# Performance work log

Hardware: AMD Instinct MI355X
Metric: run time of the kernel (lower is better)

Reference implementation:

```python
import jax, jax.numpy as jnp
import numpy as np

NBINS = 256
EARLY_STOP = 0.1  # fraction of nbins with no improvement before early break


def setup_inputs() -> dict:
    key = jax.random.key(0)
    x = jax.random.uniform(key, (8, 3, 1024, 1024), dtype=jnp.float32)
    return {"x": x}


def _otsu_forward(x):
    orig_shape = x.shape
    b, c, h, w = x.shape
    rows = b * c
    xf = x.reshape(rows, h * w)                      # (R, N) one image per row
    N = xf.shape[1]

    # Per-row shift so each row starts at 0 (mirrors `x = (x.T - min_value).T`).
    min_val = xf.min(axis=1, keepdims=True)          # (R, 1)
    xs = xf - min_val
    gmax = xs.max()                                  # global min of xs is 0, global max here
    edges = jnp.linspace(jnp.zeros((), xs.dtype), gmax, NBINS + 1)
    width = gmax / NBINS

    # Per-row histogram with torch.histc semantics over global [0, gmax].
    bin_idx = jnp.clip(jnp.floor(xs / width).astype(jnp.int32), 0, NBINS - 1)
    flat_idx = (jnp.arange(rows, dtype=jnp.int32)[:, None] * NBINS + bin_idx).reshape(-1)
    hist = jnp.bincount(flat_idx, length=rows * NBINS).reshape(rows, NBINS).astype(xs.dtype)
    cum_count = jnp.cumsum(hist, axis=1)             # px_bellow after each bin
    w0 = cum_count / N
    w1 = 1.0 - w0

    # Sorted prefix moments -> subset variances for every threshold in one pass.
    xsort = jnp.sort(xs, axis=1)
    row_mean = xs.mean(axis=1, keepdims=True)
    cvals = xsort - row_mean                         # variance is shift-invariant; centering for stability
    s1 = jnp.cumsum(cvals, axis=1)
    s2 = jnp.cumsum(cvals * cvals, axis=1)
    tot1 = s1[:, -1:]
    tot2 = s2[:, -1:]

    thresh = edges[1:]                               # bin_edges[bin+1], shape (NBINS,)
    # n0[r, bin] = #{xs[r] <= thresh[bin]}  (condition `x <= thresh` in the loop)
    n0 = jax.vmap(lambda row: jnp.searchsorted(row, thresh, side="right"))(xsort)  # (R, NBINS)

    def subset_var(S1, S2, n):
        # unbiased variance (torch.var default); nan for n <= 1 like torch
        nf = n.astype(xs.dtype)
        var = (S2 - S1 * S1 / jnp.maximum(nf, 1.0)) / jnp.maximum(nf - 1.0, 1.0)
        return jnp.where(n > 1, var, jnp.nan)

    idx0 = jnp.maximum(n0 - 1, 0)
    S1_0 = jnp.where(n0 > 0, jnp.take_along_axis(s1, idx0, axis=1), 0.0)
    S2_0 = jnp.where(n0 > 0, jnp.take_along_axis(s2, idx0, axis=1), 0.0)
    mu0 = subset_var(S1_0, S2_0, n0)                 # var of pixels <= thresh
    n1 = N - n0
    mu1 = subset_var(tot1 - S1_0, tot2 - S2_0, n1)   # var of pixels > thresh
    icv = w0 * w1 * (mu0 - mu1) ** 2                 # (R, NBINS)

    # Sequential argmax with the original's global early-stop counter.
    max_try = int(NBINS * EARLY_STOP)

    def step(carry, inputs):
        max_icv, best, no_upd, stopped = carry
        icv_b, t_b = inputs                          # (R,), scalar
        upd = (icv_b > max_icv) & jnp.logical_not(stopped)   # nan > x is False, as in torch
        max_icv = jnp.where(upd, icv_b, max_icv)
        best = jnp.where(upd, t_b, best)
        no_upd = jnp.where(jnp.any(upd), 0, no_upd + 1)
        stopped = stopped | (no_upd >= max_try)
        return (max_icv, best, no_upd, stopped), None

    init = (
        jnp.zeros(rows, xs.dtype),
        jnp.zeros(rows, xs.dtype),
        jnp.zeros((), jnp.int32),
        jnp.zeros((), jnp.bool_),
    )
    (_, best_thresh, _, _), _ = jax.lax.scan(step, init, (icv.T, thresh))

    final_thresh = best_thresh[:, None] + min_val    # back to original scale
    out = jnp.where(xf < final_thresh, jnp.zeros((), xs.dtype), xf)
    return out.reshape(orig_shape)


def reference(x):
    return _otsu_forward(x)
```

## Files before the change

### kernel.cpp

```cpp
#include <hip/hip_runtime.h>
#include <stdint.h>


#define ROWS 24
#define NPIX (1 << 20)
#define NBINS 256
#define BPR 64
#define CHUNK (NPIX / BPR)
#define MAX_TRY 25

static constexpr double kScale = 1099511627776.0;
static constexpr double Nd = 1048576.0;

#define OFF_MINNOT 0
#define OFF_MAXB   128
#define OFF_FINAL  256
#define OFF_CNT    512
#define OFF_COR    (OFF_CNT + ROWS*NBINS*4)
#define OFF_S1     (OFF_COR + ROWS*NBINS*4)
#define OFF_S2     (OFF_S1 + ROWS*NBINS*8)
#define WS_TOTAL   (OFF_S2 + ROWS*NBINS*8)

__device__ __forceinline__ double wave_gmax(const unsigned* __restrict__ minnot,
                                            const unsigned* __restrict__ maxb,
                                            int lane) {
  double d = 0.0;
  if (lane < ROWS) {
    d = (double)__uint_as_float(maxb[lane]) - (double)__uint_as_float(~minnot[lane]);
  }
  for (int o = 16; o; o >>= 1) d = fmax(d, __shfl_down(d, o));
  return d;
}

__global__ __launch_bounds__(256) void k_minmax(const float* __restrict__ x,
                                                unsigned* __restrict__ minnot,
                                                unsigned* __restrict__ maxb) {
  int row = blockIdx.x / BPR;
  int sub = blockIdx.x % BPR;
  const float4* p = (const float4*)(x + (size_t)row * NPIX + (size_t)sub * CHUNK);
  float mn = 3.4e38f, mx = 0.0f;
  for (int i = threadIdx.x; i < CHUNK / 4; i += 256) {
    float4 v = p[i];
    mn = fminf(mn, fminf(fminf(v.x, v.y), fminf(v.z, v.w)));
    mx = fmaxf(mx, fmaxf(fmaxf(v.x, v.y), fmaxf(v.z, v.w)));
  }
  __shared__ float smn[4], smx[4];
  for (int o = 32; o; o >>= 1) {
    mn = fminf(mn, __shfl_down(mn, o));
    mx = fmaxf(mx, __shfl_down(mx, o));
  }
  int wave = threadIdx.x >> 6;
  if ((threadIdx.x & 63) == 0) { smn[wave] = mn; smx[wave] = mx; }
  __syncthreads();
  if (threadIdx.x == 0) {
    for (int w = 1; w < 4; ++w) { mn = fminf(mn, smn[w]); mx = fmaxf(mx, smx[w]); }
    atomicMax(&minnot[row], ~__float_as_uint(mn));
    atomicMax(&maxb[row], __float_as_uint(mx));
  }
}

__global__ __launch_bounds__(256) void k_hist(const float* __restrict__ x,
    const unsigned* __restrict__ minnot, const unsigned* __restrict__ maxb,
    unsigned* __restrict__ gcnt, int* __restrict__ gcor,
    unsigned long long* __restrict__ gs1, unsigned long long* __restrict__ gs2) {
  __shared__ unsigned hc[NBINS];
  __shared__ int hcor[NBINS];
  __shared__ unsigned long long h1[NBINS], h2[NBINS];
  __shared__ double s_w, s_rmin;
  int t = threadIdx.x;
  hc[t] = 0u; hcor[t] = 0; h1[t] = 0ull; h2[t] = 0ull;
  int row = blockIdx.x / BPR;
  int sub = blockIdx.x % BPR;
  if (t < 64) {
    double g = wave_gmax(minnot, maxb, t);
    if (t == 0) {
      s_w = g / 256.0;
      s_rmin = (double)__uint_as_float(~minnot[row]);
    }
  }
  __syncthreads();
  double w = s_w, rmin = s_rmin;
  const float4* p = (const float4*)(x + (size_t)row * NPIX + (size_t)sub * CHUNK);
  for (int i = threadIdx.x; i < CHUNK / 4; i += 256) {
    float4 v = p[i];
    float vv[4] = {v.x, v.y, v.z, v.w};
#pragma unroll
    for (int c = 0; c < 4; ++c) {
      double xs = (double)vv[c] - rmin;
      double q = xs / w;
      int b = (int)q;
      b = b > 255 ? 255 : b;
      double elo = (double)b * w;
      double ehi = (double)(b + 1) * w;
      int j = b;
      if (xs > ehi) { if (b < 255) j = b + 1; }
      else if (b > 0 && xs <= elo) j = b - 1;
      atomicAdd(&hc[j], 1u);
      if (j != b) {
        atomicAdd(&hcor[b], 1);
        atomicAdd(&hcor[j], -1);
      }
      unsigned long long a1 = (unsigned long long)llrint(xs * kScale);
      unsigned long long a2 = (unsigned long long)llrint(xs * xs * kScale);
      atomicAdd(&h1[j], a1);
      atomicAdd(&h2[j], a2);
    }
  }
  __syncthreads();
  atomicAdd(&gcnt[row * NBINS + t], hc[t]);
  if (hcor[t] != 0) atomicAdd(&gcor[row * NBINS + t], hcor[t]);
  atomicAdd(&gs1[row * NBINS + t], h1[t]);
  atomicAdd(&gs2[row * NBINS + t], h2[t]);
}

__global__ __launch_bounds__(1024) void k_icv_scan(
    const unsigned* __restrict__ gcnt, const int* __restrict__ gcor,
    const unsigned long long* __restrict__ gs1,
    const unsigned long long* __restrict__ gs2,
    const unsigned* __restrict__ minnot, const unsigned* __restrict__ maxb,
    double* __restrict__ finalt) {
  __shared__ double sicv[ROWS * NBINS];
  __shared__ double s_w;
  int tid = threadIdx.x;
  int wave = tid >> 6, lane = tid & 63;
  if (tid < 64) {
    double g = wave_gmax(minnot, maxb, lane);
    if (tid == 0) s_w = g / 256.0;
  }
  __syncthreads();

  const double dNAN = __builtin_nan("");
#pragma unroll
  for (int pass = 0; pass < 2; ++pass) {
    int r = (pass == 0) ? wave : 16 + wave;
    if (pass == 1 && wave >= 8) break;
    int base = r * NBINS + lane * 4;
    unsigned cj[4]; int cr[4];
    *(uint4*)cj = *(const uint4*)&gcnt[base];
    *(int4*)cr = *(const int4*)&gcor[base];
    unsigned long long s1v[4], s2v[4];
#pragma unroll
    for (int k = 0; k < 4; ++k) { s1v[k] = gs1[base + k]; s2v[k] = gs2[base + k]; }
    unsigned long long P[4], A[4], B[4];
    unsigned long long rp = 0, ra = 0, rb = 0;
#pragma unroll
    for (int k = 0; k < 4; ++k) {
      unsigned cf = cj[k] + (unsigned)cr[k];
      rp += (unsigned long long)cj[k] | ((unsigned long long)cf << 32);
      ra += s1v[k]; rb += s2v[k];
      P[k] = rp; A[k] = ra; B[k] = rb;
    }
    unsigned long long tp = rp, ta = ra, tb = rb;
    for (int o = 1; o < 64; o <<= 1) {
      unsigned long long up = __shfl_up(tp, o);
      unsigned long long ua = __shfl_up(ta, o);
      unsigned long long ub = __shfl_up(tb, o);
      if (lane >= o) { tp += up; ta += ua; tb += ub; }
    }
    unsigned long long totP = __shfl(tp, 63);
    unsigned long long totA = __shfl(ta, 63);
    unsigned long long totB = __shfl(tb, 63);
    unsigned long long ep = tp - rp, ea = ta - ra, eb = tb - rb;

    double total1 = (double)totA / kScale;
    double total2 = (double)totB / kScale;
    double mean = total1 / Nd;
    double tot1 = total1 - Nd * mean;
    double tot2 = total2 - Nd * mean * mean;
    (void)totP;
#pragma unroll
    for (int k = 0; k < 4; ++k) {
      unsigned long long Pk = P[k] + ep;
      unsigned long long cjc = Pk & 0xffffffffull;
      unsigned long long cfc = Pk >> 32;
      double n0 = (double)cjc;
      double n1 = Nd - n0;
      double s1raw = (double)(A[k] + ea) / kScale;
      double s2raw = (double)(B[k] + eb) / kScale;
      double S1 = s1raw - n0 * mean;
      double S2 = s2raw - 2.0 * mean * s1raw + n0 * mean * mean;
      double mu0 = (cjc > 1ull) ? (S2 - S1 * S1 / n0) / (n0 - 1.0) : dNAN;
      double S1b = tot1 - S1, S2b = tot2 - S2;
      double mu1 = (n1 > 1.0) ? (S2b - S1b * S1b / n1) / (n1 - 1.0) : dNAN;
      double w0 = (double)cfc / Nd, w1 = 1.0 - w0;
      double dd = mu0 - mu1;
      sicv[r * NBINS + lane * 4 + k] = w0 * w1 * dd * dd;
    }
  }
  __syncthreads();

  if (tid < 64) {
    int r = tid;
    bool active = r < ROWS;
    double w = s_w;
    double maxicv = 0.0, best = 0.0;
    int no_upd = 0;
    bool stopped = false;
    for (int t = 0; t < NBINS; ++t) {
      double v = active ? sicv[r * NBINS + t] : -1.0;
      bool upd = active && !stopped && (v > maxicv);
      if (upd) { maxicv = v; best = (double)(t + 1) * w; }
      unsigned long long bal = __ballot(upd);
      if (bal != 0ull) no_upd = 0; else ++no_upd;
      if (no_upd >= MAX_TRY) stopped = true;
    }
    if (active) finalt[r] = best + (double)__uint_as_float(~minnot[r]);
  }
}

__global__ __launch_bounds__(256) void k_out(const float* __restrict__ x,
                                             const double* __restrict__ finalt,
                                             float* __restrict__ out) {
  size_t i = (size_t)blockIdx.x * blockDim.x + threadIdx.x;
  size_t stride = (size_t)gridDim.x * blockDim.x;
  const float4* xin = (const float4*)x;
  float4* o = (float4*)out;
  size_t n4 = (size_t)ROWS * NPIX / 4;
  for (; i < n4; i += stride) {
    int row = (int)(i >> 18);
    double ft = finalt[row];
    float4 v = xin[i];
    float4 rr;
    rr.x = ((double)v.x < ft) ? 0.0f : v.x;
    rr.y = ((double)v.y < ft) ? 0.0f : v.y;
    rr.z = ((double)v.z < ft) ? 0.0f : v.z;
    rr.w = ((double)v.w < ft) ? 0.0f : v.w;
    o[i] = rr;
  }
}

extern "C" void kernel_launch(void* const* d_in, const int* in_sizes, int n_in,
                              void* d_out, int out_size, void* d_ws, size_t ws_size,
                              hipStream_t stream) {
  const float* x = (const float*)d_in[0];
  float* out = (float*)d_out;
  char* ws = (char*)d_ws;
  unsigned* minnot = (unsigned*)(ws + OFF_MINNOT);
  unsigned* maxb = (unsigned*)(ws + OFF_MAXB);
  double* finalt = (double*)(ws + OFF_FINAL);
  unsigned* gcnt = (unsigned*)(ws + OFF_CNT);
  int* gcor = (int*)(ws + OFF_COR);
  unsigned long long* gs1 = (unsigned long long*)(ws + OFF_S1);
  unsigned long long* gs2 = (unsigned long long*)(ws + OFF_S2);

  hipMemsetAsync(d_ws, 0, WS_TOTAL, stream);
  k_minmax<<<ROWS * BPR, 256, 0, stream>>>(x, minnot, maxb);
  k_hist<<<ROWS * BPR, 256, 0, stream>>>(x, minnot, maxb, gcnt, gcor, gs1, gs2);
  k_icv_scan<<<1, 1024, 0, stream>>>(gcnt, gcor, gs1, gs2, minnot, maxb, finalt);
  k_out<<<3072, 256, 0, stream>>>(x, finalt, out);
}
```

Baseline: 139.6 us.

## Accumulate bin-offset moments with packed count, reciprocal divide, and split ICV kernel

The histogram kernel now accumulates each pixel's offset from its bin's lower edge instead of raw values. The count is packed into the high bits of the first-moment atomic, removing one shared atomic per pixel. The per-pixel double division is replaced by a reciprocal multiply with an FMA correction step. The ICV computation moves from one 1024-thread block into a 24-block kernel followed by a tiny scan kernel. This cuts shared-memory atomics and double divides in the hot loop, at the cost of one extra launch and a different fixed-point precision scheme that could risk overflow.

Result: no change. 137.1 us (-1.8%).

```diff
diff --git a/kernel.cpp b/kernel.cpp
--- a/kernel.cpp
+++ b/kernel.cpp
@@ -9,7 +9,10 @@
 #define CHUNK (NPIX / BPR)
 #define MAX_TRY 25
 
-static constexpr double kScale = 1099511627776.0;
+static constexpr double kD1Scale = 17592186044416.0;
+static constexpr double kD1Inv   = 1.0 / 17592186044416.0;
+static constexpr double kD2Scale = 4503599627370496.0;
+static constexpr double kD2Inv   = 1.0 / 4503599627370496.0;
 static constexpr double Nd = 1048576.0;
 
 #define OFF_MINNOT 0
@@ -17,9 +20,10 @@
 #define OFF_FINAL  256
 #define OFF_CNT    512
 #define OFF_COR    (OFF_CNT + ROWS*NBINS*4)
-#define OFF_S1     (OFF_COR + ROWS*NBINS*4)
-#define OFF_S2     (OFF_S1 + ROWS*NBINS*8)
-#define WS_TOTAL   (OFF_S2 + ROWS*NBINS*8)
+#define OFF_D1     (OFF_COR + ROWS*NBINS*4)
+#define OFF_D2     (OFF_D1 + ROWS*NBINS*8)
+#define OFF_ICV    (OFF_D2 + ROWS*NBINS*8)
+#define WS_TOTAL   (OFF_ICV + ROWS*NBINS*8)
 
 __device__ __forceinline__ double wave_gmax(const unsigned* __restrict__ minnot,
                                             const unsigned* __restrict__ maxb,
@@ -62,13 +66,12 @@
 __global__ __launch_bounds__(256) void k_hist(const float* __restrict__ x,
     const unsigned* __restrict__ minnot, const unsigned* __restrict__ maxb,
     unsigned* __restrict__ gcnt, int* __restrict__ gcor,
-    unsigned long long* __restrict__ gs1, unsigned long long* __restrict__ gs2) {
-  __shared__ unsigned hc[NBINS];
+    unsigned long long* __restrict__ gD1, unsigned long long* __restrict__ gD2) {
+  __shared__ unsigned long long hA[NBINS], hB[NBINS];
   __shared__ int hcor[NBINS];
-  __shared__ unsigned long long h1[NBINS], h2[NBINS];
   __shared__ double s_w, s_rmin;
   int t = threadIdx.x;
-  hc[t] = 0u; hcor[t] = 0; h1[t] = 0ull; h2[t] = 0ull;
+  hA[t] = 0ull; hB[t] = 0ull; hcor[t] = 0;
   int row = blockIdx.x / BPR;
   int sub = blockIdx.x % BPR;
   if (t < 64) {
@@ -80,6 +83,7 @@
   }
   __syncthreads();
   double w = s_w, rmin = s_rmin;
+  double rw = 1.0 / w;
   const float4* p = (const float4*)(x + (size_t)row * NPIX + (size_t)sub * CHUNK);
   for (int i = threadIdx.x; i < CHUNK / 4; i += 256) {
     float4 v = p[i];
@@ -87,125 +91,119 @@
 #pragma unroll
     for (int c = 0; c < 4; ++c) {
       double xs = (double)vv[c] - rmin;
-      double q = xs / w;
+      double q1 = xs * rw;
+      double rres = fma(-q1, w, xs);
+      double q = fma(rres, rw, q1);
       int b = (int)q;
       b = b > 255 ? 255 : b;
       double elo = (double)b * w;
       double ehi = (double)(b + 1) * w;
       int j = b;
-      if (xs > ehi) { if (b < 255) j = b + 1; }
-      else if (b > 0 && xs <= elo) j = b - 1;
-      atomicAdd(&hc[j], 1u);
+      double off = elo;
+      if (xs > ehi) { if (b < 255) { j = b + 1; off = ehi; } }
+      else if (b > 0 && xs <= elo) { j = b - 1; off = (double)j * w; }
       if (j != b) {
         atomicAdd(&hcor[b], 1);
         atomicAdd(&hcor[j], -1);
       }
-      unsigned long long a1 = (unsigned long long)llrint(xs * kScale);
-      unsigned long long a2 = (unsigned long long)llrint(xs * xs * kScale);
-      atomicAdd(&h1[j], a1);
-      atomicAdd(&h2[j], a2);
+      double delta = xs - off;
+      unsigned long long d1 = (unsigned long long)llrint(delta * kD1Scale);
+      unsigned long long d2 = (unsigned long long)llrint(delta * delta * kD2Scale);
+      atomicAdd(&hA[j], (1ull << 44) | d1);
+      atomicAdd(&hB[j], d2);
     }
   }
   __syncthreads();
-  atomicAdd(&gcnt[row * NBINS + t], hc[t]);
+  unsigned long long a = hA[t];
+  unsigned c = (unsigned)(a >> 44);
+  if (c) {
+    atomicAdd(&gcnt[row * NBINS + t], c);
+    atomicAdd(&gD1[row * NBINS + t], a & ((1ull << 44) - 1ull));
+  }
+  unsigned long long b2 = hB[t];
+  if (b2) atomicAdd(&gD2[row * NBINS + t], b2);
   if (hcor[t] != 0) atomicAdd(&gcor[row * NBINS + t], hcor[t]);
-  atomicAdd(&gs1[row * NBINS + t], h1[t]);
-  atomicAdd(&gs2[row * NBINS + t], h2[t]);
-}
-
-__global__ __launch_bounds__(1024) void k_icv_scan(
-    const unsigned* __restrict__ gcnt, const int* __restrict__ gcor,
-    const unsigned long long* __restrict__ gs1,
-    const unsigned long long* __restrict__ gs2,
+}
+
+__global__ __launch_bounds__(256) void k_icv(const unsigned* __restrict__ gcnt,
+    const int* __restrict__ gcor,
+    const unsigned long long* __restrict__ gD1,
+    const unsigned long long* __restrict__ gD2,
+    const unsigned* __restrict__ minnot, const unsigned* __restrict__ maxb,
+    double* __restrict__ gicv) {
+  __shared__ double sv[NBINS], su[NBINS];
+  __shared__ unsigned scnt[NBINS], scntf[NBINS];
+  __shared__ double s_w;
+  int r = blockIdx.x, t = threadIdx.x;
+  if (t < 64) {
+    double g = wave_gmax(minnot, maxb, t);
+    if (t == 0) s_w = g / 256.0;
+  }
+  __syncthreads();
+  double w = s_w;
+  unsigned cnt = gcnt[r * NBINS + t];
+  int cor = gcor[r * NBINS + t];
+  double d1 = (double)gD1[r * NBINS + t] * kD1Inv;
+  double d2 = (double)gD2[r * NBINS + t] * kD2Inv;
+  double elo = (double)t * w;
+  scnt[t] = cnt;
+  scntf[t] = cnt + (unsigned)cor;
+  sv[t] = (double)cnt * elo + d1;
+  su[t] = (double)cnt * (elo * elo) + 2.0 * elo * d1 + d2;
+  __syncthreads();
+  for (int o = 1; o < NBINS; o <<= 1) {
+    unsigned a0 = 0, a1 = 0; double b0 = 0, b1 = 0;
+    if (t >= o) { a0 = scnt[t - o]; a1 = scntf[t - o]; b0 = sv[t - o]; b1 = su[t - o]; }
+    __syncthreads();
+    if (t >= o) { scnt[t] += a0; scntf[t] += a1; sv[t] += b0; su[t] += b1; }
+    __syncthreads();
+  }
+  const double dNAN = __builtin_nan("");
+  double total1 = sv[NBINS - 1], total2 = su[NBINS - 1];
+  double mean = total1 / Nd;
+  double tot1 = total1 - Nd * mean;
+  double tot2 = total2 - Nd * mean * mean;
+  double n0 = (double)scnt[t];
+  double n1 = Nd - n0;
+  double s1raw = sv[t], s2raw = su[t];
+  double S1 = s1raw - n0 * mean;
+  double S2 = s2raw - 2.0 * mean * s1raw + n0 * mean * mean;
+  double mu0 = (scnt[t] > 1u) ? (S2 - S1 * S1 / n0) / (n0 - 1.0) : dNAN;
+  double S1b = tot1 - S1, S2b = tot2 - S2;
+  double mu1 = (n1 > 1.0) ? (S2b - S1b * S1b / n1) / (n1 - 1.0) : dNAN;
+  double w0 = (double)scntf[t] / Nd, w1v = 1.0 - w0;
+  double dd = mu0 - mu1;
+  gicv[r * NBINS + t] = w0 * w1v * dd * dd;
+}
+
+__global__ __launch_bounds__(256) void k_scan(const double* __restrict__ gicv,
     const unsigned* __restrict__ minnot, const unsigned* __restrict__ maxb,
     double* __restrict__ finalt) {
   __shared__ double sicv[ROWS * NBINS];
   __shared__ double s_w;
   int tid = threadIdx.x;
-  int wave = tid >> 6, lane = tid & 63;
+  for (int i = tid; i < ROWS * NBINS; i += 256) sicv[i] = gicv[i];
   if (tid < 64) {
-    double g = wave_gmax(minnot, maxb, lane);
+    double g = wave_gmax(minnot, maxb, tid);
     if (tid == 0) s_w = g / 256.0;
   }
   __syncthreads();
-
-  const double dNAN = __builtin_nan("");
-#pragma unroll
-  for (int pass = 0; pass < 2; ++pass) {
-    int r = (pass == 0) ? wave : 16 + wave;
-    if (pass == 1 && wave >= 8) break;
-    int base = r * NBINS + lane * 4;
-    unsigned cj[4]; int cr[4];
-    *(uint4*)cj = *(const uint4*)&gcnt[base];
-    *(int4*)cr = *(const int4*)&gcor[base];
-    unsigned long long s1v[4], s2v[4];
-#pragma unroll
-    for (int k = 0; k < 4; ++k) { s1v[k] = gs1[base + k]; s2v[k] = gs2[base + k]; }
-    unsigned long long P[4], A[4], B[4];
-    unsigned long long rp = 0, ra = 0, rb = 0;
-#pragma unroll
-    for (int k = 0; k < 4; ++k) {
-      unsigned cf = cj[k] + (unsigned)cr[k];
-      rp += (unsigned long long)cj[k] | ((unsigned long long)cf << 32);
-      ra += s1v[k]; rb += s2v[k];
-      P[k] = rp; A[k] = ra; B[k] = rb;
-    }
-    unsigned long long tp = rp, ta = ra, tb = rb;
-    for (int o = 1; o < 64; o <<= 1) {
-      unsigned long long up = __shfl_up(tp, o);
-      unsigned long long ua = __shfl_up(ta, o);
-      unsigned long long ub = __shfl_up(tb, o);
-      if (lane >= o) { tp += up; ta += ua; tb += ub; }
-    }
-    unsigned long long totP = __shfl(tp, 63);
-    unsigned long long totA = __shfl(ta, 63);
-    unsigned long long totB = __shfl(tb, 63);
-    unsigned long long ep = tp - rp, ea = ta - ra, eb = tb - rb;
-
-    double total1 = (double)totA / kScale;
-    double total2 = (double)totB / kScale;
-    double mean = total1 / Nd;
-    double tot1 = total1 - Nd * mean;
-    double tot2 = total2 - Nd * mean * mean;
-    (void)totP;
-#pragma unroll
-    for (int k = 0; k < 4; ++k) {
-      unsigned long long Pk = P[k] + ep;
-      unsigned long long cjc = Pk & 0xffffffffull;
-      unsigned long long cfc = Pk >> 32;
-      double n0 = (double)cjc;
-      double n1 = Nd - n0;
-      double s1raw = (double)(A[k] + ea) / kScale;
-      double s2raw = (double)(B[k] + eb) / kScale;
-      double S1 = s1raw - n0 * mean;
-      double S2 = s2raw - 2.0 * mean * s1raw + n0 * mean * mean;
-      double mu0 = (cjc > 1ull) ? (S2 - S1 * S1 / n0) / (n0 - 1.0) : dNAN;
-      double S1b = tot1 - S1, S2b = tot2 - S2;
-      double mu1 = (n1 > 1.0) ? (S2b - S1b * S1b / n1) / (n1 - 1.0) : dNAN;
-      double w0 = (double)cfc / Nd, w1 = 1.0 - w0;
-      double dd = mu0 - mu1;
-      sicv[r * NBINS + lane * 4 + k] = w0 * w1 * dd * dd;
-    }
-  }
-  __syncthreads();
-
-  if (tid < 64) {
-    int r = tid;
-    bool active = r < ROWS;
-    double w = s_w;
-    double maxicv = 0.0, best = 0.0;
-    int no_upd = 0;
-    bool stopped = false;
-    for (int t = 0; t < NBINS; ++t) {
-      double v = active ? sicv[r * NBINS + t] : -1.0;
-      bool upd = active && !stopped && (v > maxicv);
-      if (upd) { maxicv = v; best = (double)(t + 1) * w; }
-      unsigned long long bal = __ballot(upd);
-      if (bal != 0ull) no_upd = 0; else ++no_upd;
-      if (no_upd >= MAX_TRY) stopped = true;
-    }
-    if (active) finalt[r] = best + (double)__uint_as_float(~minnot[r]);
-  }
+  if (tid >= 64) return;
+  int r = tid;
+  bool active = r < ROWS;
+  double w = s_w;
+  double maxicv = 0.0, best = 0.0;
+  int no_upd = 0;
+  bool stopped = false;
+  for (int t = 0; t < NBINS; ++t) {
+    double v = active ? sicv[r * NBINS + t] : -1.0;
+    bool upd = active && !stopped && (v > maxicv);
+    if (upd) { maxicv = v; best = (double)(t + 1) * w; }
+    unsigned long long bal = __ballot(upd);
+    if (bal != 0ull) no_upd = 0; else ++no_upd;
+    if (no_upd >= MAX_TRY) stopped = true;
+  }
+  if (active) finalt[r] = best + (double)__uint_as_float(~minnot[r]);
 }
 
 __global__ __launch_bounds__(256) void k_out(const float* __restrict__ x,
@@ -240,12 +238,14 @@
   double* finalt = (double*)(ws + OFF_FINAL);
   unsigned* gcnt = (unsigned*)(ws + OFF_CNT);
   int* gcor = (int*)(ws + OFF_COR);
-  unsigned long long* gs1 = (unsigned long long*)(ws + OFF_S1);
-  unsigned long long* gs2 = (unsigned long long*)(ws + OFF_S2);
-
-  hipMemsetAsync(d_ws, 0, WS_TOTAL, stream);
+  unsigned long long* gD1 = (unsigned long long*)(ws + OFF_D1);
+  unsigned long long* gD2 = (unsigned long long*)(ws + OFF_D2);
+  double* gicv = (double*)(ws + OFF_ICV);
+
+  hipMemsetAsync(d_ws, 0, OFF_ICV, stream);
   k_minmax<<<ROWS * BPR, 256, 0, stream>>>(x, minnot, maxb);
-  k_hist<<<ROWS * BPR, 256, 0, stream>>>(x, minnot, maxb, gcnt, gcor, gs1, gs2);
-  k_icv_scan<<<1, 1024, 0, stream>>>(gcnt, gcor, gs1, gs2, minnot, maxb, finalt);
+  k_hist<<<ROWS * BPR, 256, 0, stream>>>(x, minnot, maxb, gcnt, gcor, gD1, gD2);
+  k_icv<<<ROWS, 256, 0, stream>>>(gcnt, gcor, gD1, gD2, minnot, maxb, gicv);
+  k_scan<<<1, 256, 0, stream>>>(gicv, minnot, maxb, finalt);
   k_out<<<3072, 256, 0, stream>>>(x, finalt, out);
 }
```
